# Optimization experiments

Measured on AMD Instinct MI355X. Metric: run time of the kernel, lower is better.

Reference implementation:

```python
import jax, jax.numpy as jnp
import numpy as np

DIM = 32
D = DIM - 1  # 31
MARGIN = 0.85


def _lorentz_rotation(x, r_idx, rot_w):
    # rot_w: (R, D*D) raw embedding weights; full table is orthogonalized every call
    ww = jax.nn.gelu(rot_w, approximate=False).reshape(-1, D, D)  # (R, D, D): D Householder vectors per relation
    norm2 = jnp.sum(ww * ww, axis=-1)[..., None, None]            # (R, D, 1, 1)
    H = jnp.eye(D, dtype=x.dtype) - 2.0 * (ww[..., :, None] * ww[..., None, :]) / norm2  # (R, D, D, D)
    Hs = jnp.swapaxes(H, 0, 1)                                    # (D, R, D, D): scan over the D reflections
    Iw0 = jnp.broadcast_to(jnp.eye(D, dtype=x.dtype), (rot_w.shape[0], D, D))

    def step(c, Hi):
        return jnp.matmul(c, Hi), None

    Q, _ = jax.lax.scan(step, Iw0, Hs)                            # (R, D, D) orthogonal matrices
    Qb = Q[r_idx]                                                 # (B, D, D)
    x_rot = jnp.einsum('bnd,bdc->bnc', x[..., 1:], Qb)
    return jnp.concatenate([x[..., :1], x_rot], axis=-1)


def _lorentz_boost(x, r_idx, boost_w):
    ro = jnp.tanh(boost_w[r_idx]) / DIM                           # (B, D)
    v2 = jnp.sum(ro * ro, axis=-1)[:, None, None]                 # (B, 1, 1)
    zeta = 1.0 / (jnp.sqrt(1.0 - v2) + 1e-8)
    t = x[..., :1]                                                # (B, N, 1)
    r = x[..., 1:]                                                # (B, N, D)
    rob = ro[:, None, :]                                          # (B, 1, D)
    dot = jnp.sum(r * rob, axis=-1, keepdims=True)                # (B, N, 1) = <r, r_o>
    x0 = zeta * t - zeta * dot
    xr = -zeta * t * rob + r + (zeta - 1.0) / (v2 + 1e-9) * rob * dot
    return jnp.concatenate([x0, xr], axis=-1)


def setup_inputs() -> dict:
    key = jax.random.key(0)
    ks = jax.random.split(key, 8)
    B, N, E, R = 1024, 256, 500000, 2000
    std = 1.0 / float(np.sqrt(DIM))
    return {
        'u': jax.random.randint(ks[0], (B,), 0, E),
        'r': jax.random.randint(ks[1], (B,), 0, R),
        'v': jax.random.randint(ks[2], (B, N), 0, E),
        'emb': jax.random.normal(ks[3], (E, DIM), jnp.float32) * std,
        'bias_head': jnp.zeros((E,), jnp.float32),
        'bias_tail': jnp.zeros((E,), jnp.float32),
        'head_rot_w': jax.random.normal(ks[4], (R, D * D), jnp.float32),
        'head_boost_w': jax.random.normal(ks[5], (R, D), jnp.float32),
        'tail_rot_w': jax.random.normal(ks[6], (R, D * D), jnp.float32),
        'tail_boost_w': jax.random.normal(ks[7], (R, D), jnp.float32),
    }


def reference(u, r, v, emb, bias_head, bias_tail, head_rot_w, head_boost_w, tail_rot_w, tail_boost_w):
    h = emb[u][:, None, :]                                        # (B, 1, DIM)
    t = emb[v]                                                    # (B, N, DIM)
    th = _lorentz_boost(_lorentz_rotation(h, r, head_rot_w), r, head_boost_w)
    tt = _lorentz_boost(_lorentz_rotation(t, r, tail_rot_w), r, tail_boost_w)
    d = tt - th                                                   # (B, N, DIM)
    # Lorentz inner <d,d> = -d0^2 + sum_i di^2
    mkv = jnp.sum(d * d, axis=-1) - 2.0 * d[..., 0] ** 2          # (B, N)
    return MARGIN - mkv + jnp.tanh(bias_head[u])[:, None] + jnp.tanh(bias_tail[v])
```

## Files before the change

kernel.cpp:

```cpp
#include <hip/hip_runtime.h>
#include <hip/hip_bf16.h>

#define MARGIN 0.85f

__global__ __launch_bounds__(64) void per_b_kernel(
    const int* __restrict__ u_idx, const int* __restrict__ r_idx,
    const float* __restrict__ emb,
    const float* __restrict__ bias_head,
    const float* __restrict__ head_rot_w,
    const float* __restrict__ head_boost_w,
    const float* __restrict__ tail_rot_w,
    const float* __restrict__ tail_boost_w,
    float* __restrict__ wv)
{
    __shared__ __align__(16) float ww[2 * 992];
    __shared__ __align__(16) float qh[992];
    __shared__ float hs[32], roh[32], rot[32], th[32], yv[32], tmp[32];

    const int lane = threadIdx.x;
    const int g = lane >> 5;
    const int j = lane & 31;
    const int b = blockIdx.x;
    const int r  = __builtin_amdgcn_readfirstlane(r_idx[b]);
    const int ub = __builtin_amdgcn_readfirstlane(u_idx[b]);

    for (int e = lane; e < 2 * 992; e += 64) ww[e] = 0.0f;
    if (lane < 32) hs[lane] = emb[(size_t)ub * 32 + lane];
    if (g == 0) roh[j] = (j < 31) ? tanhf(head_boost_w[(size_t)r * 31 + j]) * 0.03125f : 0.0f;
    else        rot[j] = (j < 31) ? tanhf(tail_boost_w[(size_t)r * 31 + j]) * 0.03125f : 0.0f;
    __syncthreads();

    {
        const float* rw = (g ? tail_rot_w : head_rot_w) + (size_t)r * 961;
        for (int e = j; e < 961; e += 32) {
            float xv = rw[e];
            float gv = 0.5f * xv * (1.0f + erff(xv * 0.7071067811865475f));
            int row = e / 31;
            int col = e - row * 31;
            ww[g * 992 + row * 32 + col] = gv;
        }
    }
    __syncthreads();

    float c[32];
    #pragma unroll
    for (int k = 0; k < 32; ++k) c[k] = (k == j) ? 1.0f : 0.0f;

    const float* wbase = &ww[g * 992];
    #pragma unroll 1
    for (int i = 0; i < 31; ++i) {
        const float* wi = wbase + i * 32;
        float w[32];
        float4 y4 = make_float4(0.f, 0.f, 0.f, 0.f);
        float4 n4 = make_float4(0.f, 0.f, 0.f, 0.f);
        #pragma unroll
        for (int c4 = 0; c4 < 8; ++c4) {
            float4 w4 = *reinterpret_cast<const float4*>(wi + c4 * 4);
            w[c4*4+0] = w4.x; w[c4*4+1] = w4.y; w[c4*4+2] = w4.z; w[c4*4+3] = w4.w;
            y4.x = fmaf(c[c4*4+0], w4.x, y4.x);
            y4.y = fmaf(c[c4*4+1], w4.y, y4.y);
            y4.z = fmaf(c[c4*4+2], w4.z, y4.z);
            y4.w = fmaf(c[c4*4+3], w4.w, y4.w);
            n4.x = fmaf(w4.x, w4.x, n4.x);
            n4.y = fmaf(w4.y, w4.y, n4.y);
            n4.z = fmaf(w4.z, w4.z, n4.z);
            n4.w = fmaf(w4.w, w4.w, n4.w);
        }
        float y = (y4.x + y4.y) + (y4.z + y4.w);
        float n = (n4.x + n4.y) + (n4.z + n4.w);
        float sy = (2.0f / n) * y;
        #pragma unroll
        for (int k = 0; k < 32; ++k) c[k] = fmaf(-sy, w[k], c[k]);
    }
    __syncthreads();

    if (g == 0 && j < 31) {
        #pragma unroll
        for (int c4 = 0; c4 < 8; ++c4)
            *reinterpret_cast<float4*>(&qh[j * 32 + c4 * 4]) =
                make_float4(c[c4*4+0], c[c4*4+1], c[c4*4+2], c[c4*4+3]);
    }
    __syncthreads();

    float hr = 0.0f;
    if (j < 31) {
        #pragma unroll 1
        for (int d = 0; d < 31; ++d) hr = fmaf(hs[1 + d], qh[d * 32 + j], hr);
    }
    if (g == 0) tmp[j] = (j < 31) ? hr * roh[j] : 0.0f;
    __syncthreads();

    float v2h = 0.0f, doth = 0.0f;
    #pragma unroll 1
    for (int k = 0; k < 31; ++k) { v2h = fmaf(roh[k], roh[k], v2h); doth += tmp[k]; }
    const float zh = 1.0f / (sqrtf(1.0f - v2h) + 1e-8f);
    const float ch = (zh - 1.0f) / (v2h + 1e-9f);
    const float h0 = hs[0];
    if (g == 0) {
        if (j < 31) th[1 + j] = fmaf(roh[j], ch * doth - zh * h0, hr);
        else        th[0] = zh * (h0 - doth);
    }
    __syncthreads();

    float v2t = 0.0f, dots = 0.0f;
    #pragma unroll 1
    for (int k = 0; k < 31; ++k) {
        v2t = fmaf(rot[k], rot[k], v2t);
        dots = fmaf(rot[k], th[1 + k], dots);
    }
    const float zt = 1.0f / (sqrtf(1.0f - v2t) + 1e-8f);
    const float ct = (zt - 1.0f) / (v2t + 1e-9f);
    const float th0 = th[0];
    if (g == 0) {
        if (j < 31) yv[1 + j] = 2.0f * fmaf(fmaf(zt, th0, ct * dots), rot[j], th[1 + j]);
        else        yv[0] = 2.0f * zt * (-th0 - dots);
    }
    __syncthreads();

    float* wout = wv + (size_t)b * 34;
    if (g == 1 && j < 31) {
        float wsp = 0.0f;
        #pragma unroll 1
        for (int k = 0; k < 31; ++k) wsp = fmaf(c[k], yv[1 + k], wsp);
        wout[1 + j] = wsp;
    }
    if (lane == 0) {
        wout[0] = yv[0];
        float beta = -th0 * th0;
        #pragma unroll 1
        for (int k = 0; k < 31; ++k) beta = fmaf(th[1 + k], th[1 + k], beta);
        wout[32] = MARGIN - beta + tanhf(bias_head[ub]);
        wout[33] = 0.0f;
    }
}

__global__ __launch_bounds__(256) void score_kernel(
    const int* __restrict__ v_idx,
    const float* __restrict__ emb,
    const float* __restrict__ bias_tail,
    const float* __restrict__ wv,
    float* __restrict__ out)
{
    const int b = blockIdx.x;
    const int tid = threadIdx.x;
    __shared__ __align__(16) float wl[36];
    if (tid < 33) wl[tid] = wv[(size_t)b * 34 + tid];
    else if (tid < 36) wl[tid] = 0.0f;
    __syncthreads();

    const int vi = v_idx[(size_t)b * 256 + tid];
    const float btl = bias_tail[vi];
    const float4* ep = reinterpret_cast<const float4*>(emb + (size_t)vi * 32);

    float dotw = 0.0f, qsum = 0.0f, t0 = 0.0f;
    #pragma unroll
    for (int qq = 0; qq < 8; ++qq) {
        float4 e4 = ep[qq];
        float4 w4 = *reinterpret_cast<const float4*>(&wl[qq * 4]);
        if (qq == 0) t0 = e4.x;
        dotw = fmaf(e4.x, w4.x, dotw);
        dotw = fmaf(e4.y, w4.y, dotw);
        dotw = fmaf(e4.z, w4.z, dotw);
        dotw = fmaf(e4.w, w4.w, dotw);
        qsum = fmaf(e4.x, e4.x, qsum);
        qsum = fmaf(e4.y, e4.y, qsum);
        qsum = fmaf(e4.z, e4.z, qsum);
        qsum = fmaf(e4.w, e4.w, qsum);
    }
    float score = wl[32] + dotw - qsum + 2.0f * t0 * t0 + tanhf(btl);
    out[(size_t)b * 256 + tid] = score;
}

extern "C" void kernel_launch(void* const* d_in, const int* in_sizes, int n_in,
                              void* d_out, int out_size, void* d_ws, size_t ws_size,
                              hipStream_t stream) {
    (void)n_in; (void)out_size; (void)ws_size;
    const int* u  = (const int*)d_in[0];
    const int* r  = (const int*)d_in[1];
    const int* v  = (const int*)d_in[2];
    const float* emb = (const float*)d_in[3];
    const float* bh  = (const float*)d_in[4];
    const float* bt  = (const float*)d_in[5];
    const float* hrw = (const float*)d_in[6];
    const float* hbw = (const float*)d_in[7];
    const float* trw = (const float*)d_in[8];
    const float* tbw = (const float*)d_in[9];

    const int B = in_sizes[0];

    float* wv = (float*)d_ws;

    per_b_kernel<<<B, 64, 0, stream>>>(u, r, emb, bh, hrw, hbw, trw, tbw, wv);
    score_kernel<<<B, 256, 0, stream>>>(v, emb, bt, wv, (float*)d_out);
}
```

Measured before the change: 149.6 us.

## Fuse per-batch rotation setup and scoring into one kernel with vector-space Householder application

Result: faster. 137.8 us (-7.9%).

```diff
diff --git a/kernel.cpp b/kernel.cpp
--- a/kernel.cpp
+++ b/kernel.cpp
@@ -1,195 +1,151 @@
 #include <hip/hip_runtime.h>
-#include <hip/hip_bf16.h>
 
 #define MARGIN 0.85f
 
-__global__ __launch_bounds__(64) void per_b_kernel(
+__device__ __forceinline__ float gelu_exact(float x) {
+    return 0.5f * x * (1.0f + erff(x * 0.7071067811865475f));
+}
+
+__global__ __launch_bounds__(256) void fused_kernel(
     const int* __restrict__ u_idx, const int* __restrict__ r_idx,
+    const int* __restrict__ v_idx,
     const float* __restrict__ emb,
-    const float* __restrict__ bias_head,
-    const float* __restrict__ head_rot_w,
-    const float* __restrict__ head_boost_w,
-    const float* __restrict__ tail_rot_w,
-    const float* __restrict__ tail_boost_w,
-    float* __restrict__ wv)
+    const float* __restrict__ bias_head, const float* __restrict__ bias_tail,
+    const float* __restrict__ head_rot_w, const float* __restrict__ head_boost_w,
+    const float* __restrict__ tail_rot_w, const float* __restrict__ tail_boost_w,
+    float* __restrict__ out)
 {
-    __shared__ __align__(16) float ww[2 * 992];
-    __shared__ __align__(16) float qh[992];
-    __shared__ float hs[32], roh[32], rot[32], th[32], yv[32], tmp[32];
+    __shared__ float wrow[62][33];
+    __shared__ float inv2n[62];
+    __shared__ float hsld[32];
+    __shared__ __align__(16) float wl[36];
 
-    const int lane = threadIdx.x;
-    const int g = lane >> 5;
-    const int j = lane & 31;
+    const int tid = threadIdx.x;
     const int b = blockIdx.x;
     const int r  = __builtin_amdgcn_readfirstlane(r_idx[b]);
     const int ub = __builtin_amdgcn_readfirstlane(u_idx[b]);
 
-    for (int e = lane; e < 2 * 992; e += 64) ww[e] = 0.0f;
-    if (lane < 32) hs[lane] = emb[(size_t)ub * 32 + lane];
-    if (g == 0) roh[j] = (j < 31) ? tanhf(head_boost_w[(size_t)r * 31 + j]) * 0.03125f : 0.0f;
-    else        rot[j] = (j < 31) ? tanhf(tail_boost_w[(size_t)r * 31 + j]) * 0.03125f : 0.0f;
+    const int vi = v_idx[(size_t)b * 256 + tid];
+    const float4* ep = reinterpret_cast<const float4*>(emb + (size_t)vi * 32);
+    const float4 e0 = ep[0], e1 = ep[1], e2 = ep[2], e3 = ep[3],
+                 e4 = ep[4], e5 = ep[5], e6 = ep[6], e7 = ep[7];
+    const float tb = tanhf(bias_tail[vi]);
+
+    const float* hw = head_rot_w + (size_t)r * 961;
+    const float* tw = tail_rot_w + (size_t)r * 961;
+    for (int e = tid; e < 961; e += 256) {
+        const int row = e / 31;
+        const int col = e - row * 31;
+        wrow[row][col]      = gelu_exact(hw[e]);
+        wrow[31 + row][col] = gelu_exact(tw[e]);
+    }
+    if (tid < 62) wrow[tid][31] = 0.0f;
+    if (tid < 32) hsld[tid] = emb[(size_t)ub * 32 + tid];
     __syncthreads();
 
-    {
-        const float* rw = (g ? tail_rot_w : head_rot_w) + (size_t)r * 961;
-        for (int e = j; e < 961; e += 32) {
-            float xv = rw[e];
-            float gv = 0.5f * xv * (1.0f + erff(xv * 0.7071067811865475f));
-            int row = e / 31;
-            int col = e - row * 31;
-            ww[g * 992 + row * 32 + col] = gv;
+    if (tid < 62) {
+        float n = 0.0f;
+        #pragma unroll
+        for (int k = 0; k < 31; ++k) n = fmaf(wrow[tid][k], wrow[tid][k], n);
+        inv2n[tid] = 2.0f / n;
+    }
+    __syncthreads();
+
+    if (tid < 64) {
+        const int k = tid & 31;
+        const bool act = (k < 31);
+
+        float x = act ? hsld[1 + k] : 0.0f;
+        const float h0 = hsld[0];
+        #pragma unroll
+        for (int i = 0; i < 31; ++i) {
+            const float w = wrow[i][k];
+            float p = x * w;
+            p += __shfl_xor(p, 1);
+            p += __shfl_xor(p, 2);
+            p += __shfl_xor(p, 4);
+            p += __shfl_xor(p, 8);
+            p += __shfl_xor(p, 16);
+            x = fmaf(-(p * inv2n[i]), w, x);
+        }
+
+        const float roh = act ? tanhf(head_boost_w[(size_t)r * 31 + k]) * 0.03125f : 0.0f;
+        float pv = roh * roh;
+        float pd = x * roh;
+        #pragma unroll
+        for (int m = 1; m < 32; m <<= 1) {
+            pv += __shfl_xor(pv, m);
+            pd += __shfl_xor(pd, m);
+        }
+        const float zh = 1.0f / (sqrtf(1.0f - pv) + 1e-8f);
+        const float ch = (zh - 1.0f) / (pv + 1e-9f);
+        const float th  = fmaf(roh, ch * pd - zh * h0, x);
+        const float th0 = zh * (h0 - pd);
+
+        const float rot = act ? tanhf(tail_boost_w[(size_t)r * 31 + k]) * 0.03125f : 0.0f;
+        float qv = rot * rot;
+        float qd = rot * th;
+        float qb = th * th;
+        #pragma unroll
+        for (int m = 1; m < 32; m <<= 1) {
+            qv += __shfl_xor(qv, m);
+            qd += __shfl_xor(qd, m);
+            qb += __shfl_xor(qb, m);
+        }
+        const float zt = 1.0f / (sqrtf(1.0f - qv) + 1e-8f);
+        const float ct = (zt - 1.0f) / (qv + 1e-9f);
+        float y = 2.0f * fmaf(fmaf(zt, th0, ct * qd), rot, th);
+        const float y0 = 2.0f * zt * (-th0 - qd);
+
+        #pragma unroll
+        for (int i = 30; i >= 0; --i) {
+            const float w = wrow[31 + i][k];
+            float p = y * w;
+            p += __shfl_xor(p, 1);
+            p += __shfl_xor(p, 2);
+            p += __shfl_xor(p, 4);
+            p += __shfl_xor(p, 8);
+            p += __shfl_xor(p, 16);
+            y = fmaf(-(p * inv2n[31 + i]), w, y);
+        }
+
+        if (tid < 32) {
+            if (act) wl[1 + k] = y;
+            else     wl[0] = y0;
+        }
+        if (tid == 0) {
+            const float beta = qb - th0 * th0;
+            wl[32] = MARGIN - beta + tanhf(bias_head[ub]);
         }
     }
     __syncthreads();
 
-    float c[32];
-    #pragma unroll
-    for (int k = 0; k < 32; ++k) c[k] = (k == j) ? 1.0f : 0.0f;
+    float dotw = 0.0f, qsum = 0.0f;
+    const float t0 = e0.x;
+#define ACC(EV, WI)                                                       \
+    {                                                                     \
+        const float4 wq = *reinterpret_cast<const float4*>(&wl[4 * WI]);  \
+        dotw = fmaf(EV.x, wq.x, dotw); dotw = fmaf(EV.y, wq.y, dotw);     \
+        dotw = fmaf(EV.z, wq.z, dotw); dotw = fmaf(EV.w, wq.w, dotw);     \
+        qsum = fmaf(EV.x, EV.x, qsum); qsum = fmaf(EV.y, EV.y, qsum);     \
+        qsum = fmaf(EV.z, EV.z, qsum); qsum = fmaf(EV.w, EV.w, qsum);     \
+    }
+    ACC(e0, 0) ACC(e1, 1) ACC(e2, 2) ACC(e3, 3)
+    ACC(e4, 4) ACC(e5, 5) ACC(e6, 6) ACC(e7, 7)
+#undef ACC
 
-    const float* wbase = &ww[g * 992];
-    #pragma unroll 1
-    for (int i = 0; i < 31; ++i) {
-        const float* wi = wbase + i * 32;
-        float w[32];
-        float4 y4 = make_float4(0.f, 0.f, 0.f, 0.f);
-        float4 n4 = make_float4(0.f, 0.f, 0.f, 0.f);
-        #pragma unroll
-        for (int c4 = 0; c4 < 8; ++c4) {
-            float4 w4 = *reinterpret_cast<const float4*>(wi + c4 * 4);
-            w[c4*4+0] = w4.x; w[c4*4+1] = w4.y; w[c4*4+2] = w4.z; w[c4*4+3] = w4.w;
-            y4.x = fmaf(c[c4*4+0], w4.x, y4.x);
-            y4.y = fmaf(c[c4*4+1], w4.y, y4.y);
-            y4.z = fmaf(c[c4*4+2], w4.z, y4.z);
-            y4.w = fmaf(c[c4*4+3], w4.w, y4.w);
-            n4.x = fmaf(w4.x, w4.x, n4.x);
-            n4.y = fmaf(w4.y, w4.y, n4.y);
-            n4.z = fmaf(w4.z, w4.z, n4.z);
-            n4.w = fmaf(w4.w, w4.w, n4.w);
-        }
-        float y = (y4.x + y4.y) + (y4.z + y4.w);
-        float n = (n4.x + n4.y) + (n4.z + n4.w);
-        float sy = (2.0f / n) * y;
-        #pragma unroll
-        for (int k = 0; k < 32; ++k) c[k] = fmaf(-sy, w[k], c[k]);
-    }
-    __syncthreads();
-
-    if (g == 0 && j < 31) {
-        #pragma unroll
-        for (int c4 = 0; c4 < 8; ++c4)
-            *reinterpret_cast<float4*>(&qh[j * 32 + c4 * 4]) =
-                make_float4(c[c4*4+0], c[c4*4+1], c[c4*4+2], c[c4*4+3]);
-    }
-    __syncthreads();
-
-    float hr = 0.0f;
-    if (j < 31) {
-        #pragma unroll 1
-        for (int d = 0; d < 31; ++d) hr = fmaf(hs[1 + d], qh[d * 32 + j], hr);
-    }
-    if (g == 0) tmp[j] = (j < 31) ? hr * roh[j] : 0.0f;
-    __syncthreads();
-
-    float v2h = 0.0f, doth = 0.0f;
-    #pragma unroll 1
-    for (int k = 0; k < 31; ++k) { v2h = fmaf(roh[k], roh[k], v2h); doth += tmp[k]; }
-    const float zh = 1.0f / (sqrtf(1.0f - v2h) + 1e-8f);
-    const float ch = (zh - 1.0f) / (v2h + 1e-9f);
-    const float h0 = hs[0];
-    if (g == 0) {
-        if (j < 31) th[1 + j] = fmaf(roh[j], ch * doth - zh * h0, hr);
-        else        th[0] = zh * (h0 - doth);
-    }
-    __syncthreads();
-
-    float v2t = 0.0f, dots = 0.0f;
-    #pragma unroll 1
-    for (int k = 0; k < 31; ++k) {
-        v2t = fmaf(rot[k], rot[k], v2t);
-        dots = fmaf(rot[k], th[1 + k], dots);
-    }
-    const float zt = 1.0f / (sqrtf(1.0f - v2t) + 1e-8f);
-    const float ct = (zt - 1.0f) / (v2t + 1e-9f);
-    const float th0 = th[0];
-    if (g == 0) {
-        if (j < 31) yv[1 + j] = 2.0f * fmaf(fmaf(zt, th0, ct * dots), rot[j], th[1 + j]);
-        else        yv[0] = 2.0f * zt * (-th0 - dots);
-    }
-    __syncthreads();
-
-    float* wout = wv + (size_t)b * 34;
-    if (g == 1 && j < 31) {
-        float wsp = 0.0f;
-        #pragma unroll 1
-        for (int k = 0; k < 31; ++k) wsp = fmaf(c[k], yv[1 + k], wsp);
-        wout[1 + j] = wsp;
-    }
-    if (lane == 0) {
-        wout[0] = yv[0];
-        float beta = -th0 * th0;
-        #pragma unroll 1
-        for (int k = 0; k < 31; ++k) beta = fmaf(th[1 + k], th[1 + k], beta);
-        wout[32] = MARGIN - beta + tanhf(bias_head[ub]);
-        wout[33] = 0.0f;
-    }
-}
-
-__global__ __launch_bounds__(256) void score_kernel(
-    const int* __restrict__ v_idx,
-    const float* __restrict__ emb,
-    const float* __restrict__ bias_tail,
-    const float* __restrict__ wv,
-    float* __restrict__ out)
-{
-    const int b = blockIdx.x;
-    const int tid = threadIdx.x;
-    __shared__ __align__(16) float wl[36];
-    if (tid < 33) wl[tid] = wv[(size_t)b * 34 + tid];
-    else if (tid < 36) wl[tid] = 0.0f;
-    __syncthreads();
-
-    const int vi = v_idx[(size_t)b * 256 + tid];
-    const float btl = bias_tail[vi];
-    const float4* ep = reinterpret_cast<const float4*>(emb + (size_t)vi * 32);
-
-    float dotw = 0.0f, qsum = 0.0f, t0 = 0.0f;
-    #pragma unroll
-    for (int qq = 0; qq < 8; ++qq) {
-        float4 e4 = ep[qq];
-        float4 w4 = *reinterpret_cast<const float4*>(&wl[qq * 4]);
-        if (qq == 0) t0 = e4.x;
-        dotw = fmaf(e4.x, w4.x, dotw);
-        dotw = fmaf(e4.y, w4.y, dotw);
-        dotw = fmaf(e4.z, w4.z, dotw);
-        dotw = fmaf(e4.w, w4.w, dotw);
-        qsum = fmaf(e4.x, e4.x, qsum);
-        qsum = fmaf(e4.y, e4.y, qsum);
-        qsum = fmaf(e4.z, e4.z, qsum);
-        qsum = fmaf(e4.w, e4.w, qsum);
-    }
-    float score = wl[32] + dotw - qsum + 2.0f * t0 * t0 + tanhf(btl);
-    out[(size_t)b * 256 + tid] = score;
+    out[(size_t)b * 256 + tid] = wl[32] + dotw - qsum + 2.0f * t0 * t0 + tb;
 }
 
 extern "C" void kernel_launch(void* const* d_in, const int* in_sizes, int n_in,
                               void* d_out, int out_size, void* d_ws, size_t ws_size,
                               hipStream_t stream) {
-    (void)n_in; (void)out_size; (void)ws_size;
-    const int* u  = (const int*)d_in[0];
-    const int* r  = (const int*)d_in[1];
-    const int* v  = (const int*)d_in[2];
-    const float* emb = (const float*)d_in[3];
-    const float* bh  = (const float*)d_in[4];
-    const float* bt  = (const float*)d_in[5];
-    const float* hrw = (const float*)d_in[6];
-    const float* hbw = (const float*)d_in[7];
-    const float* trw = (const float*)d_in[8];
-    const float* tbw = (const float*)d_in[9];
-
+    (void)n_in; (void)out_size; (void)d_ws; (void)ws_size;
     const int B = in_sizes[0];
-
-    float* wv = (float*)d_ws;
-
-    per_b_kernel<<<B, 64, 0, stream>>>(u, r, emb, bh, hrw, hbw, trw, tbw, wv);
-    score_kernel<<<B, 256, 0, stream>>>(v, emb, bt, wv, (float*)d_out);
+    fused_kernel<<<B, 256, 0, stream>>>(
+        (const int*)d_in[0], (const int*)d_in[1], (const int*)d_in[2],
+        (const float*)d_in[3], (const float*)d_in[4], (const float*)d_in[5],
+        (const float*)d_in[6], (const float*)d_in[7],
+        (const float*)d_in[8], (const float*)d_in[9],
+        (float*)d_out);
 }
```
